# Optimization experiments

Hardware: AMD Instinct MI355X
Metric: run time of the kernel (lower is better)

## Reference

```python
import jax, jax.numpy as jnp
import numpy as np

DIM = 1024
HEADS = 16


def setup_inputs() -> dict:
    key = jax.random.key(0)
    k1, k2, k3, k4 = jax.random.split(key, 4)
    X = jax.random.normal(k1, (4, 2048, DIM), dtype=jnp.float32)
    # torch Linear weight is [out, in]; store transposed [in, out] for x @ W
    W_qkv = jax.random.normal(k2, (DIM, 3 * DIM), dtype=jnp.float32) * (DIM ** -0.5)
    W_out = jax.random.normal(k3, (DIM, DIM), dtype=jnp.float32) * (DIM ** -0.5)
    b_out = jax.random.normal(k4, (DIM,), dtype=jnp.float32) * 0.01
    return {"X": X, "W_qkv": W_qkv, "W_out": W_out, "b_out": b_out}


def reference(X, W_qkv, W_out, b_out):
    b, t, d = X.shape
    h = HEADS
    hd = d // h
    scale = d ** -0.5  # NOTE: scales by full dim, matching the original module
    qkv = X @ W_qkv  # [b, t, 3d]
    q, k, v = jnp.split(qkv, 3, axis=-1)
    # [b, t, d] -> [b, h, t, hd]
    def to_heads(x):
        return x.reshape(b, t, h, hd).transpose(0, 2, 1, 3)
    q, k, v = to_heads(q), to_heads(k), to_heads(v)
    dots = jnp.einsum('bhid,bhjd->bhij', q, k) * scale  # [b, h, t, t]
    attn = jax.nn.softmax(dots, axis=-1)
    out = jnp.einsum('bhij,bhjd->bhid', attn, v)  # [b, h, t, hd]
    out = out.transpose(0, 2, 1, 3).reshape(b, t, d)
    return out @ W_out + b_out
```

## Files before the change

kernel.cpp:

```cpp
#include <hip/hip_runtime.h>
#include <hip/hip_bf16.h>
#include <stdint.h>

#define DIMD 1024
#define NB 4
#define NT 2048
#define NH 16
#define BT (NB*NT)
#define NQKV (3*DIMD)

typedef __attribute__((ext_vector_type(8))) __bf16 bf16x8;
typedef __attribute__((ext_vector_type(4))) __bf16 bf16x4;
typedef __attribute__((ext_vector_type(4))) float f32x4;
typedef __attribute__((ext_vector_type(16))) float f32x16;

#define MFMA16(a,b,c) __builtin_amdgcn_mfma_f32_16x16x32_bf16((a),(b),(c),0,0,0)
#define MFMA32(a,b,c) __builtin_amdgcn_mfma_f32_32x32x16_bf16((a),(b),(c),0,0,0)

#define QSCALE 0.0450842200277801f

__device__ __forceinline__ void gld16(const void* g, void* l) {
  __builtin_amdgcn_global_load_lds((const __attribute__((address_space(1))) void*)g,
                                   (__attribute__((address_space(3))) void*)l,
                                   16, 0, 0);
}

__device__ __forceinline__ unsigned pkbf(float a, float b) {
  unsigned short ua = __builtin_bit_cast(unsigned short, (__bf16)a);
  unsigned short ub = __builtin_bit_cast(unsigned short, (__bf16)b);
  return (unsigned)ua | ((unsigned)ub << 16);
}

__global__ __launch_bounds__(256) void k_cvt(const float* __restrict__ in,
                                             __bf16* __restrict__ out, int n4) {
  int i = blockIdx.x * blockDim.x + threadIdx.x;
  int st = gridDim.x * blockDim.x;
  for (; i < n4; i += st) {
    float4 v = ((const float4*)in)[i];
    bf16x4 o;
    o[0] = (__bf16)v.x; o[1] = (__bf16)v.y; o[2] = (__bf16)v.z; o[3] = (__bf16)v.w;
    ((bf16x4*)out)[i] = o;
  }
}

__global__ __launch_bounds__(256) void k_tcvt(const float* __restrict__ in,
                                              __bf16* __restrict__ out, int K, int N) {
  __shared__ __bf16 t[64][72];
  int n0 = blockIdx.x * 64, k0 = blockIdx.y * 64;
  int r = threadIdx.x >> 2, c0 = (threadIdx.x & 3) * 16;
  const float4* src = (const float4*)(in + (size_t)(k0 + r) * N + n0 + c0);
#pragma unroll
  for (int i = 0; i < 4; ++i) {
    float4 v = src[i];
    t[r][c0 + i*4 + 0] = (__bf16)v.x;
    t[r][c0 + i*4 + 1] = (__bf16)v.y;
    t[r][c0 + i*4 + 2] = (__bf16)v.z;
    t[r][c0 + i*4 + 3] = (__bf16)v.w;
  }
  __syncthreads();
  bf16x8 o0, o1;
#pragma unroll
  for (int i = 0; i < 8; ++i) o0[i] = t[c0 + i][r];
#pragma unroll
  for (int i = 0; i < 8; ++i) o1[i] = t[c0 + 8 + i][r];
  __bf16* dst = out + (size_t)(n0 + r) * K + k0 + c0;
  *(bf16x8*)dst = o0;
  *(bf16x8*)(dst + 8) = o1;
}

template<int MODE>
__global__ __launch_bounds__(256, 3) void k_gemm128(const __bf16* __restrict__ A,
                                                    const __bf16* __restrict__ Bt,
                                                    int nbx,
                                                    __bf16* __restrict__ oQK,
                                                    __bf16* __restrict__ oVt,
                                                    float* __restrict__ oF,
                                                    const float* __restrict__ bias) {
  constexpr int KK = 1024, KT = 32;
  __shared__ alignas(16) char L[3 * 16384];
  const int tid = threadIdx.x;
  const int lane = tid & 63, wid = tid >> 6;
  const int lr = lane & 15, lo = lane >> 4;
  const int wm = wid >> 1, wn = wid & 1;
  const int cpx = gridDim.x >> 3;
  const int swz = (blockIdx.x & 7) * cpx + (blockIdx.x >> 3);
  const int bx = swz % nbx, by = swz / nbx;
  const int m0 = by * 128, n0 = bx * 128;

  const char* gp[4];
  int loff[4];
#pragma unroll
  for (int j = 0; j < 4; ++j) {
    int c = j * 256 + tid;
    int isB = (c >= 512);
    int lc = c & 511;
    int row = lc >> 2, kof = (lc & 3) * 8;
    const __bf16* base = isB ? (Bt + (size_t)(n0 + row) * KK + kof)
                             : (A + (size_t)(m0 + row) * KK + kof);
    gp[j] = (const char*)base;
    loff[j] = c * 16;
  }
  auto STAGE = [&](int s) {
    char* bas = L + s * 16384;
    gld16(gp[0], bas + loff[0]); gp[0] += 64;
    gld16(gp[1], bas + loff[1]); gp[1] += 64;
    gld16(gp[2], bas + loff[2]); gp[2] += 64;
    gld16(gp[3], bas + loff[3]); gp[3] += 64;
  };

  f32x4 acc[4][4] = {};
  STAGE(0); STAGE(1);
  int xs = 2;

  for (int t = 0; t < KT; ++t) {
    if (t == KT - 1) asm volatile("s_waitcnt vmcnt(0)" ::: "memory");
    else             asm volatile("s_waitcnt vmcnt(4)" ::: "memory");
    asm volatile("s_barrier" ::: "memory");
    if (t <= KT - 3) { STAGE(xs); xs = (xs == 2) ? 0 : xs + 1; }
    const __bf16* fa = (const __bf16*)(L + (t % 3) * 16384) + (wm * 64 + lr) * 32 + lo * 8;
    const __bf16* fb = (const __bf16*)(L + (t % 3) * 16384 + 8192) + (wn * 64 + lr) * 32 + lo * 8;
    bf16x8 Af[4], Bf[4];
#pragma unroll
    for (int i = 0; i < 4; ++i) Af[i] = *(const bf16x8*)(fa + i * 512);
#pragma unroll
    for (int j = 0; j < 4; ++j) Bf[j] = *(const bf16x8*)(fb + j * 512);
    __builtin_amdgcn_s_setprio(1);
#pragma unroll
    for (int i = 0; i < 4; ++i)
#pragma unroll
      for (int j = 0; j < 4; ++j)
        acc[i][j] = MFMA16(Af[i], Bf[j], acc[i][j]);
    __builtin_amdgcn_s_setprio(0);
  }

  const int mb = m0 + wm * 64 + lo * 4;
  if (MODE == 0) {
    if (n0 < 1024) {
#pragma unroll
      for (int i = 0; i < 4; ++i)
#pragma unroll
        for (int j = 0; j < 4; ++j) {
          int col = n0 + wn * 64 + j * 16 + lr;
          int row = mb + i * 16;
#pragma unroll
          for (int r = 0; r < 4; ++r)
            oQK[(size_t)(row + r) * 2048 + col] = (__bf16)(acc[i][j][r] * QSCALE);
        }
    } else if (n0 < 2048) {
#pragma unroll
      for (int i = 0; i < 4; ++i)
#pragma unroll
        for (int j = 0; j < 4; ++j) {
          int col = n0 + wn * 64 + j * 16 + lr;
          int row = mb + i * 16;
#pragma unroll
          for (int r = 0; r < 4; ++r)
            oQK[(size_t)(row + r) * 2048 + col] = (__bf16)acc[i][j][r];
        }
    } else {
#pragma unroll
      for (int i = 0; i < 4; ++i)
#pragma unroll
        for (int j = 0; j < 4; ++j) {
          int dd = n0 - 2048 + wn * 64 + j * 16 + lr;
          int row = mb + i * 16;
          int bb = row >> 11, tt = row & 2047;
          bf16x4 pk;
#pragma unroll
          for (int r = 0; r < 4; ++r) pk[r] = (__bf16)acc[i][j][r];
          *(bf16x4*)(oVt + ((size_t)(bb << 10) + dd) * 2048 + tt) = pk;
        }
    }
  } else {
#pragma unroll
    for (int i = 0; i < 4; ++i)
#pragma unroll
      for (int j = 0; j < 4; ++j) {
        int col = n0 + wn * 64 + j * 16 + lr;
        float bv = bias[col];
        int row = mb + i * 16;
#pragma unroll
        for (int r = 0; r < 4; ++r)
          oF[(size_t)(row + r) * 1024 + col] = acc[i][j][r] + bv;
      }
  }
}

__global__ __launch_bounds__(256, 2) void k_attn(const __bf16* __restrict__ QK,
                                                 const __bf16* __restrict__ Vt,
                                                 __bf16* __restrict__ AO) {
  __shared__ alignas(16) char Lsm[3 * 18432];
  const int tid = threadIdx.x, w = tid >> 6, lane = tid & 63;
  const int l31 = lane & 31, hi = lane >> 5;
  const int P = blockIdx.x;
  const int low3 = P & 7, g = P >> 3;
  const int qc = g & 7;
  const int bh = ((g >> 3) << 3) + low3;
  const int h = bh & 15, b = bh >> 4;
  const int q0 = qc * 256 + w * 64;

  bf16x8 qfA[4], qfB[4];
  {
    const __bf16* Qb = QK + (size_t)(b * 2048 + q0 + l31) * 2048 + h * 64 + hi * 8;
#pragma unroll
    for (int dc = 0; dc < 4; ++dc) qfA[dc] = *(const bf16x8*)(Qb + dc * 16);
    Qb += (size_t)32 * 2048;
#pragma unroll
    for (int dc = 0; dc < 4; ++dc) qfB[dc] = *(const bf16x8*)(Qb + dc * 16);
  }
  const __bf16* Kg = QK + (size_t)(b * 2048) * 2048 + 1024 + h * 64;
  const __bf16* Vg = Vt + (size_t)(b * 1024 + h * 64) * 2048;

  const bool nch5 = (tid < 128);
  const char* gp[5];
  int loff[5], advB[5];
#pragma unroll
  for (int j = 0; j < 5; ++j) {
    int c = (j < 4) ? (j * 256 + tid) : (1024 + tid);
    if (c > 1151) c = 1151;
    int isV = (c >= 576);
    int lc = isV ? c - 576 : c;
    int row = lc / 9, col = lc - row * 9; if (col == 8) col = 0;
    const __bf16* gsrc = isV ? (Vg + (size_t)row * 2048 + col * 8)
                             : (Kg + (size_t)row * 2048 + col * 8);
    gp[j] = (const char*)gsrc;
    loff[j] = c * 16;
    advB[j] = isV ? 128 : 262144;
  }

  f32x16 oA0 = {0,0,0,0,0,0,0,0,0,0,0,0,0,0,0,0};
  f32x16 oA1 = {0,0,0,0,0,0,0,0,0,0,0,0,0,0,0,0};
  f32x16 oB0 = {0,0,0,0,0,0,0,0,0,0,0,0,0,0,0,0};
  f32x16 oB1 = {0,0,0,0,0,0,0,0,0,0,0,0,0,0,0,0};
  float lnA = 0.f, lnB = 0.f;

  auto STAGE = [&](int s) {
    char* bas = Lsm + s * 18432;
    gld16(gp[0], bas + loff[0]); gp[0] += advB[0];
    gld16(gp[1], bas + loff[1]); gp[1] += advB[1];
    gld16(gp[2], bas + loff[2]); gp[2] += advB[2];
    gld16(gp[3], bas + loff[3]); gp[3] += advB[3];
    if (nch5) { gld16(gp[4], bas + loff[4]); gp[4] += advB[4]; }
  };

  auto SMPACK = [&](const f32x16& s0, const f32x16& s1, unsigned pw[4][4], float& ln) {
    float p0a[16], p1a[16];
#pragma unroll
    for (int r = 0; r < 16; ++r) {
      p0a[r] = __builtin_amdgcn_exp2f(s0[r]);
      p1a[r] = __builtin_amdgcn_exp2f(s1[r]);
    }
    float sA = 0.f, sB = 0.f, sC = 0.f, sD = 0.f;
#pragma unroll
    for (int r = 0; r < 4; ++r) {
      sA += p0a[r];      sB += p0a[4 + r];
      sC += p0a[8 + r];  sD += p0a[12 + r];
      sA += p1a[r];      sB += p1a[4 + r];
      sC += p1a[8 + r];  sD += p1a[12 + r];
    }
    ln += (sA + sB) + (sC + sD);
#pragma unroll
    for (int c = 0; c < 4; ++c) {
      const float* pp = (c < 2) ? p0a : p1a;
      const int rb = (c & 1) * 8;
      unsigned A01 = pkbf(pp[rb + 0], pp[rb + 1]);
      unsigned A23 = pkbf(pp[rb + 2], pp[rb + 3]);
      unsigned A45 = pkbf(pp[rb + 4], pp[rb + 5]);
      unsigned A67 = pkbf(pp[rb + 6], pp[rb + 7]);
      asm("v_permlane32_swap_b32 %0, %1" : "+v"(A01), "+v"(A45));
      asm("v_permlane32_swap_b32 %0, %1" : "+v"(A23), "+v"(A67));
      pw[c][0] = A01; pw[c][1] = A23; pw[c][2] = A45; pw[c][3] = A67;
    }
  };

  STAGE(0); STAGE(1);
  int xc = 0, xs = 2;

  for (int t = 0; t < 32; ++t) {
    if (t == 31)   asm volatile("s_waitcnt vmcnt(0)" ::: "memory");
    else if (nch5) asm volatile("s_waitcnt vmcnt(5)" ::: "memory");
    else           asm volatile("s_waitcnt vmcnt(4)" ::: "memory");
    __builtin_amdgcn_s_barrier();
    if (t <= 29) { STAGE(xs); xs = (xs == 2) ? 0 : xs + 1; }

    const __bf16* Kl = (const __bf16*)(Lsm + xc * 18432);
    const __bf16* Vl = Kl + 4608;

    f32x16 sA0 = {0,0,0,0,0,0,0,0,0,0,0,0,0,0,0,0};
    f32x16 sA1 = {0,0,0,0,0,0,0,0,0,0,0,0,0,0,0,0};
    f32x16 sB0 = {0,0,0,0,0,0,0,0,0,0,0,0,0,0,0,0};
    f32x16 sB1 = {0,0,0,0,0,0,0,0,0,0,0,0,0,0,0,0};
    {
      bf16x8 kf[8];
#pragma unroll
      for (int dc = 0; dc < 4; ++dc)
        kf[dc] = *(const bf16x8*)(Kl + l31 * 72 + dc * 16 + hi * 8);
#pragma unroll
      for (int dc = 0; dc < 4; ++dc)
        kf[4 + dc] = *(const bf16x8*)(Kl + (32 + l31) * 72 + dc * 16 + hi * 8);
      __builtin_amdgcn_s_setprio(1);
#pragma unroll
      for (int dc = 0; dc < 4; ++dc) {
        sA0 = MFMA32(kf[dc], qfA[dc], sA0);
        sB0 = MFMA32(kf[dc], qfB[dc], sB0);
        sA1 = MFMA32(kf[4 + dc], qfA[dc], sA1);
        sB1 = MFMA32(kf[4 + dc], qfB[dc], sB1);
      }
      __builtin_amdgcn_s_setprio(0);
    }

    unsigned pwA[4][4], pwB[4][4];
    SMPACK(sA0, sA1, pwA, lnA);
    SMPACK(sB0, sB1, pwB, lnB);

    {
      bf16x8 vf[8];
#pragma unroll
      for (int c = 0; c < 4; ++c)
        vf[c] = *(const bf16x8*)(Vl + l31 * 72 + c * 16 + hi * 8);
#pragma unroll
      for (int c = 0; c < 4; ++c)
        vf[4 + c] = *(const bf16x8*)(Vl + (32 + l31) * 72 + c * 16 + hi * 8);
      __builtin_amdgcn_s_setprio(1);
#pragma unroll
      for (int c = 0; c < 4; ++c) {
        union { unsigned u[4]; bf16x8 v; } pa, pb;
        pa.u[0] = pwA[c][0]; pa.u[1] = pwA[c][1]; pa.u[2] = pwA[c][2]; pa.u[3] = pwA[c][3];
        pb.u[0] = pwB[c][0]; pb.u[1] = pwB[c][1]; pb.u[2] = pwB[c][2]; pb.u[3] = pwB[c][3];
        oA0 = MFMA32(pa.v, vf[c], oA0);
        oB0 = MFMA32(pb.v, vf[c], oB0);
        oA1 = MFMA32(pa.v, vf[4 + c], oA1);
        oB1 = MFMA32(pb.v, vf[4 + c], oB1);
      }
      __builtin_amdgcn_s_setprio(0);
    }

    xc = (xc == 2) ? 0 : xc + 1;
  }

  float lA = lnA + __shfl_xor(lnA, 32, 64);
  float lB = lnB + __shfl_xor(lnB, 32, 64);
  float invA = 1.0f / lA, invB = 1.0f / lB;
  __bf16* Ob = AO + (size_t)(b * 2048 + q0) * 1024 + h * 64;
#pragma unroll
  for (int r = 0; r < 16; ++r) {
    int qr = (r & 3) + 8 * (r >> 2) + 4 * hi;
    float ivA = __shfl(invA, qr, 64);
    float ivB = __shfl(invB, qr, 64);
    Ob[(size_t)qr * 1024 + l31] = (__bf16)(oA0[r] * ivA);
    Ob[(size_t)qr * 1024 + 32 + l31] = (__bf16)(oA1[r] * ivA);
    Ob[(size_t)(32 + qr) * 1024 + l31] = (__bf16)(oB0[r] * ivB);
    Ob[(size_t)(32 + qr) * 1024 + 32 + l31] = (__bf16)(oB1[r] * ivB);
  }
}

extern "C" void kernel_launch(void* const* d_in, const int* in_sizes, int n_in,
                              void* d_out, int out_size, void* d_ws, size_t ws_size,
                              hipStream_t stream) {
  const float* X    = (const float*)d_in[0];
  const float* Wqkv = (const float*)d_in[1];
  const float* Wout = (const float*)d_in[2];
  const float* bout = (const float*)d_in[3];
  float* out = (float*)d_out;
  char* ws = (char*)d_ws;

  __bf16* Xb  = (__bf16*)(ws);
  __bf16* Wqt = (__bf16*)(ws + 16777216);
  __bf16* Wot = (__bf16*)(ws + 23068672);
  __bf16* QKb = (__bf16*)(ws + 25165824);
  __bf16* Vtb = (__bf16*)(ws + 58720256);
  __bf16* AOb = (__bf16*)(ws + 75497472);

  k_cvt<<<2048, 256, 0, stream>>>(X, Xb, (BT * DIMD) / 4);
  k_tcvt<<<dim3(NQKV / 64, DIMD / 64), 256, 0, stream>>>(Wqkv, Wqt, DIMD, NQKV);
  k_tcvt<<<dim3(DIMD / 64, DIMD / 64), 256, 0, stream>>>(Wout, Wot, DIMD, DIMD);
  k_gemm128<0><<<1536, 256, 0, stream>>>(Xb, Wqt, 24, QKb, Vtb, nullptr, nullptr);
  k_attn<<<512, 256, 0, stream>>>(QKb, Vtb, AOb);
  k_gemm128<1><<<512, 256, 0, stream>>>(AOb, Wot, 8, nullptr, nullptr, out, bout);
}
```

Baseline: 187.4 us.

## Load K/V fragments directly from global into registers, dropping LDS staging

Removes the triple-buffered LDS pipeline (global_load_lds plus barriers) in the attention kernel and has each wave read its K and V MFMA fragments straight from global memory into registers, with the loop unrolled by two. The intent is to eliminate barrier synchronisation and LDS round-trips and to free shared memory for occupancy. In exchange, the four waves of a block each fetch the same K/V tile separately, which multiplies global/L2 traffic, and latency hiding now depends on compiler scheduling rather than explicit prefetch.

New measurement: 227.1 us. +21.2%, slower.

```diff
diff --git a/kernel.cpp b/kernel.cpp
--- a/kernel.cpp
+++ b/kernel.cpp
@@ -189,7 +189,6 @@
 __global__ __launch_bounds__(256, 2) void k_attn(const __bf16* __restrict__ QK,
                                                  const __bf16* __restrict__ Vt,
                                                  __bf16* __restrict__ AO) {
-  __shared__ alignas(16) char Lsm[3 * 18432];
   const int tid = threadIdx.x, w = tid >> 6, lane = tid & 63;
   const int l31 = lane & 31, hi = lane >> 5;
   const int P = blockIdx.x;
@@ -208,40 +207,14 @@
 #pragma unroll
     for (int dc = 0; dc < 4; ++dc) qfB[dc] = *(const bf16x8*)(Qb + dc * 16);
   }
-  const __bf16* Kg = QK + (size_t)(b * 2048) * 2048 + 1024 + h * 64;
-  const __bf16* Vg = Vt + (size_t)(b * 1024 + h * 64) * 2048;
-
-  const bool nch5 = (tid < 128);
-  const char* gp[5];
-  int loff[5], advB[5];
-#pragma unroll
-  for (int j = 0; j < 5; ++j) {
-    int c = (j < 4) ? (j * 256 + tid) : (1024 + tid);
-    if (c > 1151) c = 1151;
-    int isV = (c >= 576);
-    int lc = isV ? c - 576 : c;
-    int row = lc / 9, col = lc - row * 9; if (col == 8) col = 0;
-    const __bf16* gsrc = isV ? (Vg + (size_t)row * 2048 + col * 8)
-                             : (Kg + (size_t)row * 2048 + col * 8);
-    gp[j] = (const char*)gsrc;
-    loff[j] = c * 16;
-    advB[j] = isV ? 128 : 262144;
-  }
+  const __bf16* Kr = QK + (size_t)(b * 2048 + l31) * 2048 + 1024 + h * 64 + hi * 8;
+  const __bf16* Vr = Vt + (size_t)(b * 1024 + h * 64 + l31) * 2048 + hi * 8;
 
   f32x16 oA0 = {0,0,0,0,0,0,0,0,0,0,0,0,0,0,0,0};
   f32x16 oA1 = {0,0,0,0,0,0,0,0,0,0,0,0,0,0,0,0};
   f32x16 oB0 = {0,0,0,0,0,0,0,0,0,0,0,0,0,0,0,0};
   f32x16 oB1 = {0,0,0,0,0,0,0,0,0,0,0,0,0,0,0,0};
   float lnA = 0.f, lnB = 0.f;
-
-  auto STAGE = [&](int s) {
-    char* bas = Lsm + s * 18432;
-    gld16(gp[0], bas + loff[0]); gp[0] += advB[0];
-    gld16(gp[1], bas + loff[1]); gp[1] += advB[1];
-    gld16(gp[2], bas + loff[2]); gp[2] += advB[2];
-    gld16(gp[3], bas + loff[3]); gp[3] += advB[3];
-    if (nch5) { gld16(gp[4], bas + loff[4]); gp[4] += advB[4]; }
-  };
 
   auto SMPACK = [&](const f32x16& s0, const f32x16& s1, unsigned pw[4][4], float& ln) {
     float p0a[16], p1a[16];
@@ -273,69 +246,53 @@
     }
   };
 
-  STAGE(0); STAGE(1);
-  int xc = 0, xs = 2;
-
+#pragma unroll 2
   for (int t = 0; t < 32; ++t) {
-    if (t == 31)   asm volatile("s_waitcnt vmcnt(0)" ::: "memory");
-    else if (nch5) asm volatile("s_waitcnt vmcnt(5)" ::: "memory");
-    else           asm volatile("s_waitcnt vmcnt(4)" ::: "memory");
-    __builtin_amdgcn_s_barrier();
-    if (t <= 29) { STAGE(xs); xs = (xs == 2) ? 0 : xs + 1; }
-
-    const __bf16* Kl = (const __bf16*)(Lsm + xc * 18432);
-    const __bf16* Vl = Kl + 4608;
+    const int j0 = t * 64;
+    bf16x8 kf[8], vf[8];
+    {
+      const __bf16* kp = Kr + (size_t)j0 * 2048;
+#pragma unroll
+      for (int dc = 0; dc < 4; ++dc) kf[dc] = *(const bf16x8*)(kp + dc * 16);
+#pragma unroll
+      for (int dc = 0; dc < 4; ++dc) kf[4 + dc] = *(const bf16x8*)(kp + (size_t)32 * 2048 + dc * 16);
+      const __bf16* vp = Vr + j0;
+#pragma unroll
+      for (int c = 0; c < 4; ++c) vf[c] = *(const bf16x8*)(vp + c * 16);
+#pragma unroll
+      for (int c = 0; c < 4; ++c) vf[4 + c] = *(const bf16x8*)(vp + (size_t)32 * 2048 + c * 16);
+    }
 
     f32x16 sA0 = {0,0,0,0,0,0,0,0,0,0,0,0,0,0,0,0};
     f32x16 sA1 = {0,0,0,0,0,0,0,0,0,0,0,0,0,0,0,0};
     f32x16 sB0 = {0,0,0,0,0,0,0,0,0,0,0,0,0,0,0,0};
     f32x16 sB1 = {0,0,0,0,0,0,0,0,0,0,0,0,0,0,0,0};
-    {
-      bf16x8 kf[8];
-#pragma unroll
-      for (int dc = 0; dc < 4; ++dc)
-        kf[dc] = *(const bf16x8*)(Kl + l31 * 72 + dc * 16 + hi * 8);
-#pragma unroll
-      for (int dc = 0; dc < 4; ++dc)
-        kf[4 + dc] = *(const bf16x8*)(Kl + (32 + l31) * 72 + dc * 16 + hi * 8);
-      __builtin_amdgcn_s_setprio(1);
-#pragma unroll
-      for (int dc = 0; dc < 4; ++dc) {
-        sA0 = MFMA32(kf[dc], qfA[dc], sA0);
-        sB0 = MFMA32(kf[dc], qfB[dc], sB0);
-        sA1 = MFMA32(kf[4 + dc], qfA[dc], sA1);
-        sB1 = MFMA32(kf[4 + dc], qfB[dc], sB1);
-      }
-      __builtin_amdgcn_s_setprio(0);
-    }
+    __builtin_amdgcn_s_setprio(1);
+#pragma unroll
+    for (int dc = 0; dc < 4; ++dc) {
+      sA0 = MFMA32(kf[dc], qfA[dc], sA0);
+      sB0 = MFMA32(kf[dc], qfB[dc], sB0);
+      sA1 = MFMA32(kf[4 + dc], qfA[dc], sA1);
+      sB1 = MFMA32(kf[4 + dc], qfB[dc], sB1);
+    }
+    __builtin_amdgcn_s_setprio(0);
 
     unsigned pwA[4][4], pwB[4][4];
     SMPACK(sA0, sA1, pwA, lnA);
     SMPACK(sB0, sB1, pwB, lnB);
 
-    {
-      bf16x8 vf[8];
-#pragma unroll
-      for (int c = 0; c < 4; ++c)
-        vf[c] = *(const bf16x8*)(Vl + l31 * 72 + c * 16 + hi * 8);
-#pragma unroll
-      for (int c = 0; c < 4; ++c)
-        vf[4 + c] = *(const bf16x8*)(Vl + (32 + l31) * 72 + c * 16 + hi * 8);
-      __builtin_amdgcn_s_setprio(1);
-#pragma unroll
-      for (int c = 0; c < 4; ++c) {
-        union { unsigned u[4]; bf16x8 v; } pa, pb;
-        pa.u[0] = pwA[c][0]; pa.u[1] = pwA[c][1]; pa.u[2] = pwA[c][2]; pa.u[3] = pwA[c][3];
-        pb.u[0] = pwB[c][0]; pb.u[1] = pwB[c][1]; pb.u[2] = pwB[c][2]; pb.u[3] = pwB[c][3];
-        oA0 = MFMA32(pa.v, vf[c], oA0);
-        oB0 = MFMA32(pb.v, vf[c], oB0);
-        oA1 = MFMA32(pa.v, vf[4 + c], oA1);
-        oB1 = MFMA32(pb.v, vf[4 + c], oB1);
-      }
-      __builtin_amdgcn_s_setprio(0);
-    }
-
-    xc = (xc == 2) ? 0 : xc + 1;
+    __builtin_amdgcn_s_setprio(1);
+#pragma unroll
+    for (int c = 0; c < 4; ++c) {
+      union { unsigned u[4]; bf16x8 v; } pa, pb;
+      pa.u[0] = pwA[c][0]; pa.u[1] = pwA[c][1]; pa.u[2] = pwA[c][2]; pa.u[3] = pwA[c][3];
+      pb.u[0] = pwB[c][0]; pb.u[1] = pwB[c][1]; pb.u[2] = pwB[c][2]; pb.u[3] = pwB[c][3];
+      oA0 = MFMA32(pa.v, vf[c], oA0);
+      oB0 = MFMA32(pb.v, vf[c], oB0);
+      oA1 = MFMA32(pa.v, vf[4 + c], oA1);
+      oB1 = MFMA32(pb.v, vf[4 + c], oB1);
+    }
+    __builtin_amdgcn_s_setprio(0);
   }
 
   float lA = lnA + __shfl_xor(lnA, 32, 64);
```

## Fuse prep conversions into one kernel and XOR-swizzle attention LDS tiles

Applied to the files above, without the earlier changes.

The three input-conversion kernels are merged into a single launch so two kernel launches disappear. In attention, the padded 72-element LDS rows become unpadded 64-element rows with an XOR swizzle, which removes the fifth partial load per thread and cuts LDS use per block. The launch bound is raised to three blocks per CU so occupancy can grow. The risk is register pressure at the higher occupancy and bank conflicts if the swizzle does not match the read pattern.

New measurement: 283.8 us. +51.5%, slower.

```diff
diff --git a/kernel.cpp b/kernel.cpp
--- a/kernel.cpp
+++ b/kernel.cpp
@@ -31,41 +31,48 @@
   return (unsigned)ua | ((unsigned)ub << 16);
 }
 
-__global__ __launch_bounds__(256) void k_cvt(const float* __restrict__ in,
-                                             __bf16* __restrict__ out, int n4) {
-  int i = blockIdx.x * blockDim.x + threadIdx.x;
-  int st = gridDim.x * blockDim.x;
-  for (; i < n4; i += st) {
-    float4 v = ((const float4*)in)[i];
-    bf16x4 o;
-    o[0] = (__bf16)v.x; o[1] = (__bf16)v.y; o[2] = (__bf16)v.z; o[3] = (__bf16)v.w;
-    ((bf16x4*)out)[i] = o;
-  }
-}
-
-__global__ __launch_bounds__(256) void k_tcvt(const float* __restrict__ in,
-                                              __bf16* __restrict__ out, int K, int N) {
+__global__ __launch_bounds__(256) void k_prep(const float* __restrict__ X,
+                                              const float* __restrict__ Wqkv,
+                                              const float* __restrict__ Wout,
+                                              __bf16* __restrict__ Xb,
+                                              __bf16* __restrict__ Wqt,
+                                              __bf16* __restrict__ Wot) {
   __shared__ __bf16 t[64][72];
-  int n0 = blockIdx.x * 64, k0 = blockIdx.y * 64;
-  int r = threadIdx.x >> 2, c0 = (threadIdx.x & 3) * 16;
-  const float4* src = (const float4*)(in + (size_t)(k0 + r) * N + n0 + c0);
-#pragma unroll
-  for (int i = 0; i < 4; ++i) {
-    float4 v = src[i];
-    t[r][c0 + i*4 + 0] = (__bf16)v.x;
-    t[r][c0 + i*4 + 1] = (__bf16)v.y;
-    t[r][c0 + i*4 + 2] = (__bf16)v.z;
-    t[r][c0 + i*4 + 3] = (__bf16)v.w;
-  }
-  __syncthreads();
-  bf16x8 o0, o1;
-#pragma unroll
-  for (int i = 0; i < 8; ++i) o0[i] = t[c0 + i][r];
-#pragma unroll
-  for (int i = 0; i < 8; ++i) o1[i] = t[c0 + 8 + i][r];
-  __bf16* dst = out + (size_t)(n0 + r) * K + k0 + c0;
-  *(bf16x8*)dst = o0;
-  *(bf16x8*)(dst + 8) = o1;
+  const int bid = blockIdx.x, tid = threadIdx.x;
+  if (bid < 1024) {
+    const float* in; __bf16* out; int K, N, n0, k0;
+    if (bid < 768) { in = Wqkv; out = Wqt; K = 1024; N = 3072; n0 = (bid % 48) * 64; k0 = (bid / 48) * 64; }
+    else { int id = bid - 768; in = Wout; out = Wot; K = 1024; N = 1024; n0 = (id % 16) * 64; k0 = (id / 16) * 64; }
+    int r = tid >> 2, c0 = (tid & 3) * 16;
+    const float4* src = (const float4*)(in + (size_t)(k0 + r) * N + n0 + c0);
+#pragma unroll
+    for (int i = 0; i < 4; ++i) {
+      float4 v = src[i];
+      t[r][c0 + i*4 + 0] = (__bf16)v.x;
+      t[r][c0 + i*4 + 1] = (__bf16)v.y;
+      t[r][c0 + i*4 + 2] = (__bf16)v.z;
+      t[r][c0 + i*4 + 3] = (__bf16)v.w;
+    }
+    __syncthreads();
+    bf16x8 o0, o1;
+#pragma unroll
+    for (int i = 0; i < 8; ++i) o0[i] = t[c0 + i][r];
+#pragma unroll
+    for (int i = 0; i < 8; ++i) o1[i] = t[c0 + 8 + i][r];
+    __bf16* dst = out + (size_t)(n0 + r) * K + k0 + c0;
+    *(bf16x8*)dst = o0;
+    *(bf16x8*)(dst + 8) = o1;
+  } else {
+    const int n4 = (BT * DIMD) / 4;
+    int i = (bid - 1024) * 256 + tid;
+    const int st = 2048 * 256;
+    for (; i < n4; i += st) {
+      float4 v = ((const float4*)X)[i];
+      bf16x4 o;
+      o[0] = (__bf16)v.x; o[1] = (__bf16)v.y; o[2] = (__bf16)v.z; o[3] = (__bf16)v.w;
+      ((bf16x4*)Xb)[i] = o;
+    }
+  }
 }
 
 template<int MODE>
@@ -186,10 +193,10 @@
   }
 }
 
-__global__ __launch_bounds__(256, 2) void k_attn(const __bf16* __restrict__ QK,
+__global__ __launch_bounds__(256, 3) void k_attn(const __bf16* __restrict__ QK,
                                                  const __bf16* __restrict__ Vt,
                                                  __bf16* __restrict__ AO) {
-  __shared__ alignas(16) char Lsm[3 * 18432];
+  __shared__ alignas(16) char Lsm[3 * 16384];
   const int tid = threadIdx.x, w = tid >> 6, lane = tid & 63;
   const int l31 = lane & 31, hi = lane >> 5;
   const int P = blockIdx.x;
@@ -211,22 +218,28 @@
   const __bf16* Kg = QK + (size_t)(b * 2048) * 2048 + 1024 + h * 64;
   const __bf16* Vg = Vt + (size_t)(b * 1024 + h * 64) * 2048;
 
-  const bool nch5 = (tid < 128);
-  const char* gp[5];
-  int loff[5], advB[5];
-#pragma unroll
-  for (int j = 0; j < 5; ++j) {
-    int c = (j < 4) ? (j * 256 + tid) : (1024 + tid);
-    if (c > 1151) c = 1151;
-    int isV = (c >= 576);
-    int lc = isV ? c - 576 : c;
-    int row = lc / 9, col = lc - row * 9; if (col == 8) col = 0;
-    const __bf16* gsrc = isV ? (Vg + (size_t)row * 2048 + col * 8)
-                             : (Kg + (size_t)row * 2048 + col * 8);
+  const char* gp[4];
+  int loff[4], advB[4];
+#pragma unroll
+  for (int j = 0; j < 4; ++j) {
+    int c = j * 256 + tid;
+    int isV = (c >= 512);
+    int lc = c & 511;
+    int r = lc >> 3, s = lc & 7;
+    int colc = s ^ (r & 7);
+    const __bf16* gsrc = isV ? (Vg + (size_t)r * 2048 + colc * 8)
+                             : (Kg + (size_t)r * 2048 + colc * 8);
     gp[j] = (const char*)gsrc;
     loff[j] = c * 16;
     advB[j] = isV ? 128 : 262144;
   }
+
+  int koff[8];
+#pragma unroll
+  for (int h0 = 0; h0 < 2; ++h0)
+#pragma unroll
+    for (int dc = 0; dc < 4; ++dc)
+      koff[h0 * 4 + dc] = (h0 * 32 + l31) * 64 + (((2 * dc + hi) ^ (l31 & 7)) * 8);
 
   f32x16 oA0 = {0,0,0,0,0,0,0,0,0,0,0,0,0,0,0,0};
   f32x16 oA1 = {0,0,0,0,0,0,0,0,0,0,0,0,0,0,0,0};
@@ -235,12 +248,11 @@
   float lnA = 0.f, lnB = 0.f;
 
   auto STAGE = [&](int s) {
-    char* bas = Lsm + s * 18432;
+    char* bas = Lsm + s * 16384;
     gld16(gp[0], bas + loff[0]); gp[0] += advB[0];
     gld16(gp[1], bas + loff[1]); gp[1] += advB[1];
     gld16(gp[2], bas + loff[2]); gp[2] += advB[2];
     gld16(gp[3], bas + loff[3]); gp[3] += advB[3];
-    if (nch5) { gld16(gp[4], bas + loff[4]); gp[4] += advB[4]; }
   };
 
   auto SMPACK = [&](const f32x16& s0, const f32x16& s1, unsigned pw[4][4], float& ln) {
@@ -277,14 +289,13 @@
   int xc = 0, xs = 2;
 
   for (int t = 0; t < 32; ++t) {
-    if (t == 31)   asm volatile("s_waitcnt vmcnt(0)" ::: "memory");
-    else if (nch5) asm volatile("s_waitcnt vmcnt(5)" ::: "memory");
-    else           asm volatile("s_waitcnt vmcnt(4)" ::: "memory");
+    if (t == 31) asm volatile("s_waitcnt vmcnt(0)" ::: "memory");
+    else         asm volatile("s_waitcnt vmcnt(4)" ::: "memory");
     __builtin_amdgcn_s_barrier();
     if (t <= 29) { STAGE(xs); xs = (xs == 2) ? 0 : xs + 1; }
 
-    const __bf16* Kl = (const __bf16*)(Lsm + xc * 18432);
-    const __bf16* Vl = Kl + 4608;
+    const __bf16* Kl = (const __bf16*)(Lsm + xc * 16384);
+    const __bf16* Vl = Kl + 4096;
 
     f32x16 sA0 = {0,0,0,0,0,0,0,0,0,0,0,0,0,0,0,0};
     f32x16 sA1 = {0,0,0,0,0,0,0,0,0,0,0,0,0,0,0,0};
@@ -293,11 +304,7 @@
     {
       bf16x8 kf[8];
 #pragma unroll
-      for (int dc = 0; dc < 4; ++dc)
-        kf[dc] = *(const bf16x8*)(Kl + l31 * 72 + dc * 16 + hi * 8);
-#pragma unroll
-      for (int dc = 0; dc < 4; ++dc)
-        kf[4 + dc] = *(const bf16x8*)(Kl + (32 + l31) * 72 + dc * 16 + hi * 8);
+      for (int i = 0; i < 8; ++i) kf[i] = *(const bf16x8*)(Kl + koff[i]);
       __builtin_amdgcn_s_setprio(1);
 #pragma unroll
       for (int dc = 0; dc < 4; ++dc) {
@@ -316,11 +323,7 @@
     {
       bf16x8 vf[8];
 #pragma unroll
-      for (int c = 0; c < 4; ++c)
-        vf[c] = *(const bf16x8*)(Vl + l31 * 72 + c * 16 + hi * 8);
-#pragma unroll
-      for (int c = 0; c < 4; ++c)
-        vf[4 + c] = *(const bf16x8*)(Vl + (32 + l31) * 72 + c * 16 + hi * 8);
+      for (int i = 0; i < 8; ++i) vf[i] = *(const bf16x8*)(Vl + koff[i]);
       __builtin_amdgcn_s_setprio(1);
 #pragma unroll
       for (int c = 0; c < 4; ++c) {
@@ -371,9 +374,7 @@
   __bf16* Vtb = (__bf16*)(ws + 58720256);
   __bf16* AOb = (__bf16*)(ws + 75497472);
 
-  k_cvt<<<2048, 256, 0, stream>>>(X, Xb, (BT * DIMD) / 4);
-  k_tcvt<<<dim3(NQKV / 64, DIMD / 64), 256, 0, stream>>>(Wqkv, Wqt, DIMD, NQKV);
-  k_tcvt<<<dim3(DIMD / 64, DIMD / 64), 256, 0, stream>>>(Wout, Wot, DIMD, DIMD);
+  k_prep<<<3072, 256, 0, stream>>>(X, Wqkv, Wout, Xb, Wqt, Wot);
   k_gemm128<0><<<1536, 256, 0, stream>>>(Xb, Wqt, 24, QKb, Vtb, nullptr, nullptr);
   k_attn<<<512, 256, 0, stream>>>(QKb, Vtb, AOb);
   k_gemm128<1><<<512, 256, 0, stream>>>(AOb, Wot, 8, nullptr, nullptr, out, bout);
```
